# Kernel optimization log

Hardware: AMD Instinct MI355X
Metric: run time of the kernel (lower is better)

Reference implementation:

```python
import jax, jax.numpy as jnp
import numpy as np

B, T, L = 4096, 26, 4      # batch, num sparse tables, bag size (multi-hot)
N_ROWS, M = 100000, 64     # rows per table, embedding dim
LN_BOT = [13, 512, 256, 64]
LN_TOP = [415, 512, 256, 1]


def _mlp_params(key, ln):
    Ws, bs = [], []
    for i in range(len(ln) - 1):
        n, m = ln[i], ln[i + 1]
        key, k1, k2 = jax.random.split(key, 3)
        Ws.append(jax.random.normal(k1, (m, n), jnp.float32) * np.sqrt(2.0 / (m + n)))
        bs.append(jax.random.normal(k2, (m,), jnp.float32) * np.sqrt(1.0 / m))
    return Ws, bs


def setup_inputs() -> dict:
    key = jax.random.key(0)
    k_dense, k_idx, k_emb, k_bot, k_top = jax.random.split(key, 5)
    dense_x = jax.random.normal(k_dense, (B, LN_BOT[0]), jnp.float32)
    sparse_idx = jax.random.randint(k_idx, (B, T, L), 0, N_ROWS, jnp.int64 if jax.config.jax_enable_x64 else jnp.int32)
    # per-table uniform init U(-1/sqrt(n), 1/sqrt(n)); all tables same size -> stacked
    bound = np.sqrt(1.0 / N_ROWS)
    emb_tables = jax.random.uniform(k_emb, (T, N_ROWS, M), jnp.float32, -bound, bound)
    bw, bb = _mlp_params(k_bot, LN_BOT)
    tw, tb = _mlp_params(k_top, LN_TOP)
    return {
        "dense_x": dense_x, "sparse_idx": sparse_idx, "emb_tables": emb_tables,
        "bot_W0": bw[0], "bot_b0": bb[0], "bot_W1": bw[1], "bot_b1": bb[1],
        "bot_W2": bw[2], "bot_b2": bb[2],
        "top_W0": tw[0], "top_b0": tb[0], "top_W1": tw[1], "top_b1": tb[1],
        "top_W2": tw[2], "top_b2": tb[2],
    }


def _dlrm_forward(dense_x, sparse_idx, emb_tables, bot, top):
    # bottom MLP (all ReLU; sigmoid_layer index not hit for bottom)
    x = dense_x
    for W, b in bot:
        x = jax.nn.relu(x @ W.T + b)                       # [B, 64] at the end
    # apply_emb: per-table EmbeddingBag(mode='sum'): gather L rows, sum-pool
    # emb_tables: [T, N, M], sparse_idx: [B, T, L] -> E: [B, T, M]
    E = jax.vmap(lambda tab, ix: tab[ix].sum(axis=1), in_axes=(0, 1), out_axes=1)(
        emb_tables, sparse_idx)
    # dot interaction: concat bottom output with pooled embeddings
    Tcat = jnp.concatenate([x[:, None, :], E], axis=1)     # [B, T+1, M]
    Z = jnp.einsum("bim,bjm->bij", Tcat, Tcat)             # [B, T+1, T+1]
    li, lj = np.tril_indices(T + 1, k=-1)                  # strictly lower triangle
    Zflat = Z[:, li, lj]                                   # [B, (T+1)T/2]
    R = jnp.concatenate([x, Zflat], axis=1)                # [B, 415]
    # top MLP: ReLU hidden, Sigmoid on last layer
    h = R
    for i, (W, b) in enumerate(top):
        h = h @ W.T + b
        h = jax.nn.sigmoid(h) if i == len(top) - 1 else jax.nn.relu(h)
    return h                                               # [B, 1]


def reference(dense_x, sparse_idx, emb_tables,
              bot_W0, bot_b0, bot_W1, bot_b1, bot_W2, bot_b2,
              top_W0, top_b0, top_W1, top_b1, top_W2, top_b2):
    bot = [(bot_W0, bot_b0), (bot_W1, bot_b1), (bot_W2, bot_b2)]
    top = [(top_W0, top_b0), (top_W1, top_b1), (top_W2, top_b2)]
    return _dlrm_forward(dense_x, sparse_idx, emb_tables, bot, top)
```

## Files before the change

### kernel.cpp

```cpp
#include <hip/hip_runtime.h>
#include <hip/hip_bf16.h>
#include <cstddef>
#include <cstdint>

#define BATCH 4096
#define TT 26
#define LL 4
#define NROWS 100000
#define MM 64
#define RSTR 512

typedef __attribute__((ext_vector_type(8))) short bf16x8;
typedef __attribute__((ext_vector_type(4))) float f32x4;
typedef __attribute__((ext_vector_type(16))) float f32x16;

#define AS1 __attribute__((address_space(1)))
#define AS3 __attribute__((address_space(3)))

__device__ __forceinline__ void gload_lds16(const void* g, void* l) {
    __builtin_amdgcn_global_load_lds((const AS1 unsigned int*)g,
                                     (AS3 unsigned int*)l, 16, 0, 0);
}

__device__ __forceinline__ float bu2f(unsigned short u) {
    unsigned int x = (unsigned int)u << 16;
    float f; __builtin_memcpy(&f, &x, 4); return f;
}

#define GATB 4096
#define BOT0B 8192
__global__ __launch_bounds__(256) void fused_front_kernel(
    const int* __restrict__ idx, const float* __restrict__ emb,
    const float* __restrict__ dense, const float* __restrict__ bw0,
    const float* __restrict__ bb0,
    const float* __restrict__ bw1, const float* __restrict__ bw2,
    const float* __restrict__ tw0, const float* __restrict__ tw1,
    unsigned short* __restrict__ E, __hip_bfloat16* __restrict__ x1,
    __hip_bfloat16* __restrict__ bw1b, __hip_bfloat16* __restrict__ bw2b,
    __hip_bfloat16* __restrict__ tw0b, __hip_bfloat16* __restrict__ tw1b)
{
    __shared__ int sidx[TT * LL];
    __shared__ float xr[13];
    const int tid = threadIdx.x;

    if (blockIdx.x < GATB) {
        const int b = blockIdx.x;
        const int lane = tid & 63;
        const int w = tid >> 6;
        if (tid < TT * LL) sidx[tid] = idx[(size_t)b * (TT * LL) + tid];
        __syncthreads();
        float v[7][4];
#pragma unroll
        for (int rr = 0; rr < 7; rr++) {
            int t = rr * 4 + w;
            if (t < TT) {
                const float* tab = emb + (size_t)t * NROWS * MM + lane;
#pragma unroll
                for (int l = 0; l < LL; l++)
                    v[rr][l] = tab[(size_t)sidx[t * LL + l] * MM];
            }
        }
#pragma unroll
        for (int rr = 0; rr < 7; rr++) {
            int t = rr * 4 + w;
            if (t < TT) {
                float s = v[rr][0] + v[rr][1] + v[rr][2] + v[rr][3];
                __hip_bfloat16 hv = __float2bfloat16(s);
                E[(size_t)b * (TT * MM) + t * MM + lane] = *(unsigned short*)&hv;
            }
        }
        return;
    }
    if (blockIdx.x < BOT0B) {
        const int b = blockIdx.x - GATB;
        if (tid < 13) xr[tid] = dense[b * 13 + tid];
        __syncthreads();
        for (int j = tid; j < 512; j += 256) {
            const float* w = bw0 + j * 13;
            float s = bb0[j];
#pragma unroll
            for (int k = 0; k < 13; k++) s = fmaf(xr[k], w[k], s);
            x1[(size_t)b * 512 + j] = __float2bfloat16(fmaxf(s, 0.f));
        }
        return;
    }
    {
        int i = (blockIdx.x - BOT0B) * 256 + tid;
        if (i < 131072) {
            bw1b[i] = __float2bfloat16(bw1[i]);
        } else if (i < 147456) {
            int j = i - 131072; bw2b[j] = __float2bfloat16(bw2[j]);
        } else if (i < 409600) {
            int j = i - 147456; int n = j >> 9, k = j & 511;
            tw0b[j] = __float2bfloat16(k < 415 ? tw0[n * 415 + k] : 0.f);
        } else if (i < 540672) {
            int j = i - 409600; tw1b[j] = __float2bfloat16(tw1[j]);
        }
    }
}

template<int KK, int ACT>
__global__ __launch_bounds__(256, 2) void gemm_db(
    const __hip_bfloat16* __restrict__ A,
    const __hip_bfloat16* __restrict__ W,
    const float* __restrict__ bias,
    __hip_bfloat16* __restrict__ C, int ldc)
{
    constexpr int KSTEPS = KK / 128;
    __shared__ __align__(16) short As[2][64 * 128];
    __shared__ __align__(16) short Bs[2][64 * 128];

    const int tid  = threadIdx.x;
    const int lane = tid & 63;
    const int wid  = tid >> 6;
    const int wr   = wid >> 1, wc = wid & 1;

    const char* Ab = (const char*)A + (size_t)blockIdx.x * (64 * KK * 2);
    const char* Wb = (const char*)W + (size_t)blockIdx.y * (64 * KK * 2);

    auto stage = [&](const char* Gb, char* Ls, int ks) {
#pragma unroll
        for (int j = 0; j < 4; j++) {
            int ci  = j * 256 + tid;
            int row = ci >> 4;
            int cb  = (ci & 15) * 16;
            int src = row * (2 * KK) + ks * 256 + (cb ^ ((row & 7) << 4));
            gload_lds16(Gb + src, Ls + row * 256 + cb);
        }
    };

    const int fr  = lane & 15;
    const int fkb = (lane >> 4) * 16;
    const int xrr = (fr & 7) << 4;
    const int oA0 = (wr * 32 + fr) * 256;
    const int oA1 = oA0 + 16 * 256;
    const int oB0 = (wc * 32 + fr) * 256;
    const int oB1 = oB0 + 16 * 256;

    f32x4 acc[2][2] = {};

    auto compute = [&](const char* Ah, const char* Bh) {
#pragma unroll
        for (int kf = 0; kf < 4; kf++) {
            int pc = (kf * 64 + fkb) ^ xrr;
            bf16x8 a0 = *(const bf16x8*)(Ah + oA0 + pc);
            bf16x8 a1 = *(const bf16x8*)(Ah + oA1 + pc);
            bf16x8 b0 = *(const bf16x8*)(Bh + oB0 + pc);
            bf16x8 b1 = *(const bf16x8*)(Bh + oB1 + pc);
            acc[0][0] = __builtin_amdgcn_mfma_f32_16x16x32_bf16(a0, b0, acc[0][0], 0, 0, 0);
            acc[0][1] = __builtin_amdgcn_mfma_f32_16x16x32_bf16(a0, b1, acc[0][1], 0, 0, 0);
            acc[1][0] = __builtin_amdgcn_mfma_f32_16x16x32_bf16(a1, b0, acc[1][0], 0, 0, 0);
            acc[1][1] = __builtin_amdgcn_mfma_f32_16x16x32_bf16(a1, b1, acc[1][1], 0, 0, 0);
        }
    };

    stage(Ab, (char*)As[0], 0); stage(Wb, (char*)Bs[0], 0);
    stage(Ab, (char*)As[1], 1); stage(Wb, (char*)Bs[1], 1);

#pragma unroll
    for (int ks = 0; ks < KSTEPS; ks++) {
        if (ks < KSTEPS - 1) { asm volatile("s_waitcnt vmcnt(8)" ::: "memory"); }
        else                 { asm volatile("s_waitcnt vmcnt(0)" ::: "memory"); }
        __builtin_amdgcn_sched_barrier(0);
        __builtin_amdgcn_s_barrier();
        __builtin_amdgcn_sched_barrier(0);
        compute((const char*)As[ks & 1], (const char*)Bs[ks & 1]);
        __builtin_amdgcn_sched_barrier(0);
        if (ks + 2 < KSTEPS) {
            __builtin_amdgcn_s_barrier();
            stage(Ab, (char*)As[ks & 1], ks + 2);
            stage(Wb, (char*)Bs[ks & 1], ks + 2);
        }
    }

    const int col0 = blockIdx.y * 64 + wc * 32 + (lane & 15);
    const int row0 = blockIdx.x * 64 + wr * 32 + (lane >> 4) * 4;
    float bias_n0 = bias[col0];
    float bias_n1 = bias[col0 + 16];
#pragma unroll
    for (int mi = 0; mi < 2; mi++) {
#pragma unroll
        for (int j = 0; j < 4; j++) {
            int row = row0 + mi * 16 + j;
            float v0 = acc[mi][0][j] + bias_n0;
            float v1 = acc[mi][1][j] + bias_n1;
            if (ACT == 1) { v0 = fmaxf(v0, 0.f); v1 = fmaxf(v1, 0.f); }
            C[(size_t)row * ldc + col0]      = __float2bfloat16(v0);
            C[(size_t)row * ldc + col0 + 16] = __float2bfloat16(v1);
        }
    }
}

__global__ __launch_bounds__(256) void interact_kernel(
    const unsigned short* __restrict__ E, __hip_bfloat16* __restrict__ R)
{
    __shared__ __align__(16) char T[4][32 * 128];
    const int tid = threadIdx.x;
    const int lane = tid & 63;
    const int w = tid >> 6;
    const int b = blockIdx.x * 4 + w;
    char* Tw = T[w];
    const unsigned short* Eb = E + (size_t)b * (TT * MM);
    const unsigned short* Xb = (const unsigned short*)R + (size_t)b * RSTR;

#pragma unroll
    for (int i = 0; i < 7; i++) {
        int id = i * 64 + lane;
        if (id < 432) {
            int r = id >> 4, c4 = (id & 15) * 4;
            const unsigned short* src = (r == 0) ? (Xb + c4) : (Eb + (r - 1) * 64 + c4);
            ushort4 val = *(const ushort4*)src;
            *(ushort4*)(Tw + r * 128 + ((c4 * 2) ^ ((r & 7) << 4))) = val;
        }
    }
#pragma unroll
    for (int i = 0; i < 2; i++) {
        int id = i * 64 + lane;
        if (id < 80) {
            int r = 27 + (id >> 4), c4 = (id & 15) * 4;
            *(ushort4*)(Tw + r * 128 + ((c4 * 2) ^ ((r & 7) << 4))) = (ushort4){0, 0, 0, 0};
        }
    }
    __syncthreads();

    f32x16 acc = {};
#pragma unroll
    for (int m = 0; m < 4; m++) {
        int byteoff = (lane & 31) * 128 + ((m * 32 + (lane >> 5) * 16) ^ ((lane & 7) << 4));
        bf16x8 f = *(const bf16x8*)(Tw + byteoff);
        acc = __builtin_amdgcn_mfma_f32_32x32x16_bf16(f, f, acc, 0, 0, 0);
    }
    __hip_bfloat16* Rb = R + (size_t)b * RSTR;
    const int col = lane & 31;
#pragma unroll
    for (int q = 0; q < 4; q++) {
#pragma unroll
        for (int j = 0; j < 4; j++) {
            int row = j + 8 * q + 4 * (lane >> 5);
            if (row < 27 && col < row)
                Rb[64 + row * (row - 1) / 2 + col] = __float2bfloat16(acc[q * 4 + j]);
        }
    }
    for (int p = lane; p < 97; p += 64)
        Rb[415 + p] = __float2bfloat16(0.f);
}

__global__ __launch_bounds__(256) void top2_kernel(
    const __hip_bfloat16* __restrict__ h, const float* __restrict__ W,
    const float* __restrict__ bias, float* __restrict__ out)
{
    __shared__ float ws[256];
    int tid = threadIdx.x;
    ws[tid] = W[tid];
    __syncthreads();
    int b = blockIdx.x * 4 + (tid >> 6);
    int lane = tid & 63;
    const unsigned short* hb = (const unsigned short*)(h + (size_t)b * 256);
    ushort4 hv = *(const ushort4*)&hb[lane * 4];
    float4 wv = *(const float4*)&ws[lane * 4];
    float s = bu2f(hv.x) * wv.x + bu2f(hv.y) * wv.y + bu2f(hv.z) * wv.z + bu2f(hv.w) * wv.w;
#pragma unroll
    for (int off = 32; off >= 1; off >>= 1)
        s += __shfl_xor(s, off, 64);
    if (lane == 0) {
        float v = s + bias[0];
        out[b] = 1.0f / (1.0f + expf(-v));
    }
}

extern "C" void kernel_launch(void* const* d_in, const int* in_sizes, int n_in,
                              void* d_out, int out_size, void* d_ws, size_t ws_size,
                              hipStream_t stream) {
    const float* dense = (const float*)d_in[0];
    const int*   sidx  = (const int*)d_in[1];
    const float* emb   = (const float*)d_in[2];
    const float* bw0   = (const float*)d_in[3];
    const float* bb0   = (const float*)d_in[4];
    const float* bw1   = (const float*)d_in[5];
    const float* bb1   = (const float*)d_in[6];
    const float* bw2   = (const float*)d_in[7];
    const float* bb2   = (const float*)d_in[8];
    const float* tw0   = (const float*)d_in[9];
    const float* tb0   = (const float*)d_in[10];
    const float* tw1   = (const float*)d_in[11];
    const float* tb1   = (const float*)d_in[12];
    const float* tw2   = (const float*)d_in[13];
    const float* tb2   = (const float*)d_in[14];
    float* out = (float*)d_out;

    char* wsb = (char*)d_ws;
    unsigned short* E    = (unsigned short*)(wsb);
    __hip_bfloat16* R    = (__hip_bfloat16*)(wsb + (16u << 20));
    __hip_bfloat16* h1   = (__hip_bfloat16*)(wsb + (20u << 20));
    __hip_bfloat16* h2   = (__hip_bfloat16*)(wsb + (24u << 20));
    __hip_bfloat16* x1   = (__hip_bfloat16*)(wsb + (26u << 20));
    __hip_bfloat16* x2   = (__hip_bfloat16*)(wsb + (30u << 20));
    __hip_bfloat16* bw1b = (__hip_bfloat16*)(wsb + (32u << 20));
    __hip_bfloat16* bw2b = bw1b + 131072;
    __hip_bfloat16* tw0b = bw2b + 16384;
    __hip_bfloat16* tw1b = tw0b + 262144;

    fused_front_kernel<<<GATB + BATCH + 2112, 256, 0, stream>>>(
        sidx, emb, dense, bw0, bb0, bw1, bw2, tw0, tw1,
        E, x1, bw1b, bw2b, tw0b, tw1b);

    gemm_db<512, 1><<<dim3(64, 4), 256, 0, stream>>>(x1, bw1b, bb1, x2, 256);

    gemm_db<256, 1><<<dim3(64, 1), 256, 0, stream>>>(x2, bw2b, bb2, R, RSTR);

    interact_kernel<<<BATCH / 4, 256, 0, stream>>>(E, R);

    gemm_db<512, 1><<<dim3(64, 8), 256, 0, stream>>>(R, tw0b, tb0, h1, 512);

    gemm_db<512, 1><<<dim3(64, 4), 256, 0, stream>>>(h1, tw1b, tb1, h2, 256);

    top2_kernel<<<BATCH / 4, 256, 0, stream>>>(h2, tw2, tb2, out);
}
```

Measured before the change: 56.79 us.

## Fuse embedding Gram into gather, fuse bottom-MLP tail with x-dot products, full-K GEMMs

The gather blocks now stage the pooled embeddings in LDS and compute the embedding-embedding dot products with one MFMA wave, writing them directly into R. The last bottom-MLP GEMM also computes the x·E dot products from LDS, so the separate interaction kernel is gone. Two GEMMs switch to a full-K variant that stages all of K into LDS up front with two barriers instead of a K loop. Together these remove a kernel launch and a re-read of E from global memory. In exchange the gather blocks use more LDS and barriers, the bottom GEMM runs on only 64 blocks, and the larger full-K LDS footprint may lower occupancy.

```diff
diff --git a/kernel.cpp b/kernel.cpp
--- a/kernel.cpp
+++ b/kernel.cpp
@@ -37,8 +37,10 @@
     const float* __restrict__ tw0, const float* __restrict__ tw1,
     unsigned short* __restrict__ E, __hip_bfloat16* __restrict__ x1,
     __hip_bfloat16* __restrict__ bw1b, __hip_bfloat16* __restrict__ bw2b,
-    __hip_bfloat16* __restrict__ tw0b, __hip_bfloat16* __restrict__ tw1b)
+    __hip_bfloat16* __restrict__ tw0b, __hip_bfloat16* __restrict__ tw1b,
+    __hip_bfloat16* __restrict__ R)
 {
+    __shared__ __align__(16) char T[32 * 128];
     __shared__ int sidx[TT * LL];
     __shared__ float xr[13];
     const int tid = threadIdx.x;
@@ -48,7 +50,14 @@
         const int lane = tid & 63;
         const int w = tid >> 6;
         if (tid < TT * LL) sidx[tid] = idx[(size_t)b * (TT * LL) + tid];
+        for (int i = tid; i < 6 * 64; i += 256) {
+            int rid = i >> 6;
+            int r = rid ? (26 + rid) : 0;
+            int l = i & 63;
+            *(short*)(T + r * 128 + ((l * 2) ^ ((r & 7) << 4))) = 0;
+        }
         __syncthreads();
+
         float v[7][4];
 #pragma unroll
         for (int rr = 0; rr < 7; rr++) {
@@ -66,7 +75,36 @@
             if (t < TT) {
                 float s = v[rr][0] + v[rr][1] + v[rr][2] + v[rr][3];
                 __hip_bfloat16 hv = __float2bfloat16(s);
+                int r = t + 1;
+                *(short*)(T + r * 128 + ((lane * 2) ^ ((r & 7) << 4))) = *(short*)&hv;
                 E[(size_t)b * (TT * MM) + t * MM + lane] = *(unsigned short*)&hv;
+            }
+        }
+        __syncthreads();
+
+        __hip_bfloat16* Rb = R + (size_t)b * RSTR;
+        if (w == 1) {
+            Rb[415 + lane] = __float2bfloat16(0.f);
+            if (lane < 33) Rb[479 + lane] = __float2bfloat16(0.f);
+        }
+        if (w == 0) {
+            f32x16 acc = {};
+#pragma unroll
+            for (int m = 0; m < 4; m++) {
+                int byteoff = (lane & 31) * 128 +
+                              ((m * 32 + (lane >> 5) * 16) ^ ((lane & 7) << 4));
+                bf16x8 f = *(const bf16x8*)(T + byteoff);
+                acc = __builtin_amdgcn_mfma_f32_32x32x16_bf16(f, f, acc, 0, 0, 0);
+            }
+            const int col = lane & 31;
+#pragma unroll
+            for (int q = 0; q < 4; q++) {
+#pragma unroll
+                for (int j = 0; j < 4; j++) {
+                    int row = j + 8 * q + 4 * (lane >> 5);
+                    if (row < 27 && col >= 1 && col < row)
+                        Rb[64 + row * (row - 1) / 2 + col] = __float2bfloat16(acc[q * 4 + j]);
+                }
             }
         }
         return;
@@ -95,6 +133,211 @@
             tw0b[j] = __float2bfloat16(k < 415 ? tw0[n * 415 + k] : 0.f);
         } else if (i < 540672) {
             int j = i - 409600; tw1b[j] = __float2bfloat16(tw1[j]);
+        }
+    }
+}
+
+template<int KK, int ACT>
+__global__ __launch_bounds__(256) void gemm_fullk(
+    const __hip_bfloat16* __restrict__ A,
+    const __hip_bfloat16* __restrict__ W,
+    const float* __restrict__ bias,
+    __hip_bfloat16* __restrict__ C, int ldc)
+{
+    constexpr int HS   = KK / 2;
+    constexpr int CPRH = KK / 16;
+    constexpr int NI   = (64 * CPRH) / 256;
+    __shared__ __align__(16) short As0[64 * HS];
+    __shared__ __align__(16) short As1[64 * HS];
+    __shared__ __align__(16) short Bs0[64 * HS];
+    __shared__ __align__(16) short Bs1[64 * HS];
+
+    const int tid  = threadIdx.x;
+    const int lane = tid & 63;
+    const int wid  = tid >> 6;
+    const int wr   = wid >> 1, wc = wid & 1;
+
+    const char* Ab = (const char*)A + (size_t)blockIdx.x * (64 * KK * 2);
+    const char* Wb = (const char*)W + (size_t)blockIdx.y * (64 * KK * 2);
+
+    auto stage = [&](const char* Gb, short* Ls, int h) {
+#pragma unroll
+        for (int j = 0; j < NI; j++) {
+            int ci  = j * 256 + tid;
+            int row = ci / CPRH;
+            int cb  = (ci & (CPRH - 1)) * 16;
+            int src = row * (2 * KK) + h * KK + (cb ^ ((row & 7) << 4));
+            gload_lds16(Gb + src, (char*)Ls + row * KK + cb);
+        }
+    };
+    stage(Ab, As0, 0); stage(Wb, Bs0, 0);
+    stage(Ab, As1, 1); stage(Wb, Bs1, 1);
+
+    const int frow = lane & 15;
+    const int fkb  = (lane >> 4) * 16;
+    const int xr   = (frow & 7) << 4;
+    const int oA0  = (wr * 32 + frow) * KK;
+    const int oA1  = oA0 + 16 * KK;
+    const int oB0  = (wc * 32 + frow) * KK;
+    const int oB1  = oB0 + 16 * KK;
+
+    f32x4 acc[2][2] = {};
+
+    auto compute = [&](const short* Ah, const short* Bh) {
+#pragma unroll
+        for (int ks = 0; ks < KK / 64; ks++) {
+            int pc = (ks * 64 + fkb) ^ xr;
+            bf16x8 a0 = *(const bf16x8*)((const char*)Ah + oA0 + pc);
+            bf16x8 a1 = *(const bf16x8*)((const char*)Ah + oA1 + pc);
+            bf16x8 b0 = *(const bf16x8*)((const char*)Bh + oB0 + pc);
+            bf16x8 b1 = *(const bf16x8*)((const char*)Bh + oB1 + pc);
+            acc[0][0] = __builtin_amdgcn_mfma_f32_16x16x32_bf16(a0, b0, acc[0][0], 0, 0, 0);
+            acc[0][1] = __builtin_amdgcn_mfma_f32_16x16x32_bf16(a0, b1, acc[0][1], 0, 0, 0);
+            acc[1][0] = __builtin_amdgcn_mfma_f32_16x16x32_bf16(a1, b0, acc[1][0], 0, 0, 0);
+            acc[1][1] = __builtin_amdgcn_mfma_f32_16x16x32_bf16(a1, b1, acc[1][1], 0, 0, 0);
+        }
+    };
+
+    asm volatile("s_waitcnt vmcnt(%0)" :: "i"(2 * NI) : "memory");
+    __builtin_amdgcn_sched_barrier(0);
+    __builtin_amdgcn_s_barrier();
+    __builtin_amdgcn_sched_barrier(0);
+    compute(As0, Bs0);
+    asm volatile("s_waitcnt vmcnt(0)" ::: "memory");
+    __builtin_amdgcn_sched_barrier(0);
+    __builtin_amdgcn_s_barrier();
+    __builtin_amdgcn_sched_barrier(0);
+    compute(As1, Bs1);
+
+    const int col0 = blockIdx.y * 64 + wc * 32 + (lane & 15);
+    const int row0 = blockIdx.x * 64 + wr * 32 + (lane >> 4) * 4;
+    float bias_n0 = bias[col0];
+    float bias_n1 = bias[col0 + 16];
+#pragma unroll
+    for (int mi = 0; mi < 2; mi++) {
+#pragma unroll
+        for (int j = 0; j < 4; j++) {
+            int row = row0 + mi * 16 + j;
+            float v0 = acc[mi][0][j] + bias_n0;
+            float v1 = acc[mi][1][j] + bias_n1;
+            if (ACT == 1) { v0 = fmaxf(v0, 0.f); v1 = fmaxf(v1, 0.f); }
+            C[(size_t)row * ldc + col0]      = __float2bfloat16(v0);
+            C[(size_t)row * ldc + col0 + 16] = __float2bfloat16(v1);
+        }
+    }
+}
+
+__global__ __launch_bounds__(256) void bot2_gram_kernel(
+    const __hip_bfloat16* __restrict__ A,
+    const __hip_bfloat16* __restrict__ W,
+    const float* __restrict__ bias,
+    const unsigned short* __restrict__ E,
+    __hip_bfloat16* __restrict__ R)
+{
+    constexpr int KK = 256;
+    __shared__ __align__(16) short As0[64 * 128];
+    __shared__ __align__(16) short As1[64 * 128];
+    __shared__ __align__(16) short Bs0[64 * 128];
+    __shared__ __align__(16) short Bs1[64 * 128];
+    __shared__ unsigned short x3L[64 * 64];
+
+    const int tid  = threadIdx.x;
+    const int lane = tid & 63;
+    const int wid  = tid >> 6;
+    const int wr   = wid >> 1, wc = wid & 1;
+
+    const char* Ab = (const char*)A + (size_t)blockIdx.x * (64 * KK * 2);
+    const char* Wb = (const char*)W;
+
+    auto stage = [&](const char* Gb, short* Ls, int h) {
+#pragma unroll
+        for (int j = 0; j < 4; j++) {
+            int ci  = j * 256 + tid;
+            int row = ci >> 4;
+            int cb  = (ci & 15) * 16;
+            int src = row * (2 * KK) + h * KK + (cb ^ ((row & 7) << 4));
+            gload_lds16(Gb + src, (char*)Ls + row * KK + cb);
+        }
+    };
+    stage(Ab, As0, 0); stage(Wb, Bs0, 0);
+    stage(Ab, As1, 1); stage(Wb, Bs1, 1);
+
+    const int frow = lane & 15;
+    const int fkb  = (lane >> 4) * 16;
+    const int xr   = (frow & 7) << 4;
+    const int oA0  = (wr * 32 + frow) * KK;
+    const int oA1  = oA0 + 16 * KK;
+    const int oB0  = (wc * 32 + frow) * KK;
+    const int oB1  = oB0 + 16 * KK;
+
+    f32x4 acc[2][2] = {};
+    auto compute = [&](const short* Ah, const short* Bh) {
+#pragma unroll
+        for (int ks = 0; ks < KK / 64; ks++) {
+            int pc = (ks * 64 + fkb) ^ xr;
+            bf16x8 a0 = *(const bf16x8*)((const char*)Ah + oA0 + pc);
+            bf16x8 a1 = *(const bf16x8*)((const char*)Ah + oA1 + pc);
+            bf16x8 b0 = *(const bf16x8*)((const char*)Bh + oB0 + pc);
+            bf16x8 b1 = *(const bf16x8*)((const char*)Bh + oB1 + pc);
+            acc[0][0] = __builtin_amdgcn_mfma_f32_16x16x32_bf16(a0, b0, acc[0][0], 0, 0, 0);
+            acc[0][1] = __builtin_amdgcn_mfma_f32_16x16x32_bf16(a0, b1, acc[0][1], 0, 0, 0);
+            acc[1][0] = __builtin_amdgcn_mfma_f32_16x16x32_bf16(a1, b0, acc[1][0], 0, 0, 0);
+            acc[1][1] = __builtin_amdgcn_mfma_f32_16x16x32_bf16(a1, b1, acc[1][1], 0, 0, 0);
+        }
+    };
+
+    asm volatile("s_waitcnt vmcnt(8)" ::: "memory");
+    __builtin_amdgcn_sched_barrier(0);
+    __builtin_amdgcn_s_barrier();
+    __builtin_amdgcn_sched_barrier(0);
+    compute(As0, Bs0);
+    asm volatile("s_waitcnt vmcnt(0)" ::: "memory");
+    __builtin_amdgcn_sched_barrier(0);
+    __builtin_amdgcn_s_barrier();
+    __builtin_amdgcn_sched_barrier(0);
+    compute(As1, Bs1);
+
+    const int col0 = wc * 32 + (lane & 15);
+    const int lrow0 = wr * 32 + (lane >> 4) * 4;
+    const int row0 = blockIdx.x * 64 + lrow0;
+    float bias_n0 = bias[col0];
+    float bias_n1 = bias[col0 + 16];
+#pragma unroll
+    for (int mi = 0; mi < 2; mi++) {
+#pragma unroll
+        for (int j = 0; j < 4; j++) {
+            int row = row0 + mi * 16 + j;
+            int lr  = lrow0 + mi * 16 + j;
+            float v0 = fmaxf(acc[mi][0][j] + bias_n0, 0.f);
+            float v1 = fmaxf(acc[mi][1][j] + bias_n1, 0.f);
+            __hip_bfloat16 h0 = __float2bfloat16(v0);
+            __hip_bfloat16 h1 = __float2bfloat16(v1);
+            R[(size_t)row * RSTR + col0]      = h0;
+            R[(size_t)row * RSTR + col0 + 16] = h1;
+            x3L[lr * 64 + col0]      = *(unsigned short*)&h0;
+            x3L[lr * 64 + col0 + 16] = *(unsigned short*)&h1;
+        }
+    }
+    __syncthreads();
+
+    const int b0 = blockIdx.x * 64;
+#pragma unroll
+    for (int k = 0; k < 7; k++) {
+        int job = tid + k * 256;
+        if (job < 1664) {
+            int bl = job / 26;
+            int i  = job - bl * 26 + 1;
+            const unsigned short* Er = E + ((size_t)(b0 + bl) * TT + (i - 1)) * MM;
+            const unsigned short* xrow = &x3L[bl * 64];
+            float s = 0.f;
+#pragma unroll
+            for (int c = 0; c < 64; c += 4) {
+                ushort4 e4 = *(const ushort4*)&Er[c];
+                ushort4 x4 = *(const ushort4*)&xrow[c];
+                s += bu2f(e4.x) * bu2f(x4.x) + bu2f(e4.y) * bu2f(x4.y)
+                   + bu2f(e4.z) * bu2f(x4.z) + bu2f(e4.w) * bu2f(x4.w);
+            }
+            R[(size_t)(b0 + bl) * RSTR + 64 + i * (i - 1) / 2] = __float2bfloat16(s);
         }
     }
 }
@@ -189,60 +432,6 @@
             C[(size_t)row * ldc + col0 + 16] = __float2bfloat16(v1);
         }
     }
-}
-
-__global__ __launch_bounds__(256) void interact_kernel(
-    const unsigned short* __restrict__ E, __hip_bfloat16* __restrict__ R)
-{
-    __shared__ __align__(16) char T[4][32 * 128];
-    const int tid = threadIdx.x;
-    const int lane = tid & 63;
-    const int w = tid >> 6;
-    const int b = blockIdx.x * 4 + w;
-    char* Tw = T[w];
-    const unsigned short* Eb = E + (size_t)b * (TT * MM);
-    const unsigned short* Xb = (const unsigned short*)R + (size_t)b * RSTR;
-
-#pragma unroll
-    for (int i = 0; i < 7; i++) {
-        int id = i * 64 + lane;
-        if (id < 432) {
-            int r = id >> 4, c4 = (id & 15) * 4;
-            const unsigned short* src = (r == 0) ? (Xb + c4) : (Eb + (r - 1) * 64 + c4);
-            ushort4 val = *(const ushort4*)src;
-            *(ushort4*)(Tw + r * 128 + ((c4 * 2) ^ ((r & 7) << 4))) = val;
-        }
-    }
-#pragma unroll
-    for (int i = 0; i < 2; i++) {
-        int id = i * 64 + lane;
-        if (id < 80) {
-            int r = 27 + (id >> 4), c4 = (id & 15) * 4;
-            *(ushort4*)(Tw + r * 128 + ((c4 * 2) ^ ((r & 7) << 4))) = (ushort4){0, 0, 0, 0};
-        }
-    }
-    __syncthreads();
-
-    f32x16 acc = {};
-#pragma unroll
-    for (int m = 0; m < 4; m++) {
-        int byteoff = (lane & 31) * 128 + ((m * 32 + (lane >> 5) * 16) ^ ((lane & 7) << 4));
-        bf16x8 f = *(const bf16x8*)(Tw + byteoff);
-        acc = __builtin_amdgcn_mfma_f32_32x32x16_bf16(f, f, acc, 0, 0, 0);
-    }
-    __hip_bfloat16* Rb = R + (size_t)b * RSTR;
-    const int col = lane & 31;
-#pragma unroll
-    for (int q = 0; q < 4; q++) {
-#pragma unroll
-        for (int j = 0; j < 4; j++) {
-            int row = j + 8 * q + 4 * (lane >> 5);
-            if (row < 27 && col < row)
-                Rb[64 + row * (row - 1) / 2 + col] = __float2bfloat16(acc[q * 4 + j]);
-        }
-    }
-    for (int p = lane; p < 97; p += 64)
-        Rb[415 + p] = __float2bfloat16(0.f);
 }
 
 __global__ __launch_bounds__(256) void top2_kernel(
@@ -302,17 +491,15 @@
 
     fused_front_kernel<<<GATB + BATCH + 2112, 256, 0, stream>>>(
         sidx, emb, dense, bw0, bb0, bw1, bw2, tw0, tw1,
-        E, x1, bw1b, bw2b, tw0b, tw1b);
-
-    gemm_db<512, 1><<<dim3(64, 4), 256, 0, stream>>>(x1, bw1b, bb1, x2, 256);
-
-    gemm_db<256, 1><<<dim3(64, 1), 256, 0, stream>>>(x2, bw2b, bb2, R, RSTR);
-
-    interact_kernel<<<BATCH / 4, 256, 0, stream>>>(E, R);
+        E, x1, bw1b, bw2b, tw0b, tw1b, R);
+
+    gemm_fullk<512, 1><<<dim3(64, 4), 256, 0, stream>>>(x1, bw1b, bb1, x2, 256);
+
+    bot2_gram_kernel<<<64, 256, 0, stream>>>(x2, bw2b, bb2, E, R);
 
     gemm_db<512, 1><<<dim3(64, 8), 256, 0, stream>>>(R, tw0b, tb0, h1, 512);
 
-    gemm_db<512, 1><<<dim3(64, 4), 256, 0, stream>>>(h1, tw1b, tb1, h2, 256);
+    gemm_fullk<512, 1><<<dim3(64, 4), 256, 0, stream>>>(h1, tw1b, tb1, h2, 256);
 
     top2_kernel<<<BATCH / 4, 256, 0, stream>>>(h2, tw2, tb2, out);
 }
```

Result: slower. 59.17 us (+4.2%).

## Add full-K single-shot GEMM kernel staging whole K into LDS in two halves

Applied to the files above, without the earlier changes.

Introduces gemm_fullk, which issues async global-to-LDS loads for the entire K extent of A and W tiles up front, split into two halves. It computes on the first half while the second is still landing, replacing the k-step double-buffered loop of gemm_db. This is applied to three of the small MLP GEMMs. It aims to cut per-k-step barrier and loop overhead for these short GEMMs, at the cost of much larger LDS use (128KB for K=512), which lowers occupancy.

```diff
diff --git a/kernel.cpp b/kernel.cpp
--- a/kernel.cpp
+++ b/kernel.cpp
@@ -95,6 +95,96 @@
             tw0b[j] = __float2bfloat16(k < 415 ? tw0[n * 415 + k] : 0.f);
         } else if (i < 540672) {
             int j = i - 409600; tw1b[j] = __float2bfloat16(tw1[j]);
+        }
+    }
+}
+
+template<int KK, int ACT>
+__global__ __launch_bounds__(256) void gemm_fullk(
+    const __hip_bfloat16* __restrict__ A,
+    const __hip_bfloat16* __restrict__ W,
+    const float* __restrict__ bias,
+    __hip_bfloat16* __restrict__ C, int ldc)
+{
+    constexpr int HS   = KK / 2;
+    constexpr int CPRH = KK / 16;
+    constexpr int NI   = (64 * CPRH) / 256;
+    __shared__ __align__(16) short As0[64 * HS];
+    __shared__ __align__(16) short As1[64 * HS];
+    __shared__ __align__(16) short Bs0[64 * HS];
+    __shared__ __align__(16) short Bs1[64 * HS];
+
+    const int tid  = threadIdx.x;
+    const int lane = tid & 63;
+    const int wid  = tid >> 6;
+    const int wr   = wid >> 1, wc = wid & 1;
+
+    const char* Ab = (const char*)A + (size_t)blockIdx.x * (64 * KK * 2);
+    const char* Wb = (const char*)W + (size_t)blockIdx.y * (64 * KK * 2);
+
+    auto stage = [&](const char* Gb, short* Ls, int h) {
+#pragma unroll
+        for (int j = 0; j < NI; j++) {
+            int ci  = j * 256 + tid;
+            int row = ci / CPRH;
+            int cb  = (ci & (CPRH - 1)) * 16;
+            int src = row * (2 * KK) + h * KK + (cb ^ ((row & 7) << 4));
+            gload_lds16(Gb + src, (char*)Ls + row * KK + cb);
+        }
+    };
+    stage(Ab, As0, 0); stage(Wb, Bs0, 0);
+    stage(Ab, As1, 1); stage(Wb, Bs1, 1);
+
+    const int frow = lane & 15;
+    const int fkb  = (lane >> 4) * 16;
+    const int xr   = (frow & 7) << 4;
+    const int oA0  = (wr * 32 + frow) * KK;
+    const int oA1  = oA0 + 16 * KK;
+    const int oB0  = (wc * 32 + frow) * KK;
+    const int oB1  = oB0 + 16 * KK;
+
+    f32x4 acc[2][2] = {};
+
+    auto compute = [&](const short* Ah, const short* Bh) {
+#pragma unroll
+        for (int ks = 0; ks < KK / 64; ks++) {
+            int pc = (ks * 64 + fkb) ^ xr;
+            bf16x8 a0 = *(const bf16x8*)((const char*)Ah + oA0 + pc);
+            bf16x8 a1 = *(const bf16x8*)((const char*)Ah + oA1 + pc);
+            bf16x8 b0 = *(const bf16x8*)((const char*)Bh + oB0 + pc);
+            bf16x8 b1 = *(const bf16x8*)((const char*)Bh + oB1 + pc);
+            acc[0][0] = __builtin_amdgcn_mfma_f32_16x16x32_bf16(a0, b0, acc[0][0], 0, 0, 0);
+            acc[0][1] = __builtin_amdgcn_mfma_f32_16x16x32_bf16(a0, b1, acc[0][1], 0, 0, 0);
+            acc[1][0] = __builtin_amdgcn_mfma_f32_16x16x32_bf16(a1, b0, acc[1][0], 0, 0, 0);
+            acc[1][1] = __builtin_amdgcn_mfma_f32_16x16x32_bf16(a1, b1, acc[1][1], 0, 0, 0);
+        }
+    };
+
+    asm volatile("s_waitcnt vmcnt(%0)" :: "i"(2 * NI) : "memory");
+    __builtin_amdgcn_sched_barrier(0);
+    __builtin_amdgcn_s_barrier();
+    __builtin_amdgcn_sched_barrier(0);
+    compute(As0, Bs0);
+    asm volatile("s_waitcnt vmcnt(0)" ::: "memory");
+    __builtin_amdgcn_sched_barrier(0);
+    __builtin_amdgcn_s_barrier();
+    __builtin_amdgcn_sched_barrier(0);
+    compute(As1, Bs1);
+
+    const int col0 = blockIdx.y * 64 + wc * 32 + (lane & 15);
+    const int row0 = blockIdx.x * 64 + wr * 32 + (lane >> 4) * 4;
+    float bias_n0 = bias[col0];
+    float bias_n1 = bias[col0 + 16];
+#pragma unroll
+    for (int mi = 0; mi < 2; mi++) {
+#pragma unroll
+        for (int j = 0; j < 4; j++) {
+            int row = row0 + mi * 16 + j;
+            float v0 = acc[mi][0][j] + bias_n0;
+            float v1 = acc[mi][1][j] + bias_n1;
+            if (ACT == 1) { v0 = fmaxf(v0, 0.f); v1 = fmaxf(v1, 0.f); }
+            C[(size_t)row * ldc + col0]      = __float2bfloat16(v0);
+            C[(size_t)row * ldc + col0 + 16] = __float2bfloat16(v1);
         }
     }
 }
@@ -304,15 +394,15 @@
         sidx, emb, dense, bw0, bb0, bw1, bw2, tw0, tw1,
         E, x1, bw1b, bw2b, tw0b, tw1b);
 
-    gemm_db<512, 1><<<dim3(64, 4), 256, 0, stream>>>(x1, bw1b, bb1, x2, 256);
-
-    gemm_db<256, 1><<<dim3(64, 1), 256, 0, stream>>>(x2, bw2b, bb2, R, RSTR);
+    gemm_fullk<512, 1><<<dim3(64, 4), 256, 0, stream>>>(x1, bw1b, bb1, x2, 256);
+
+    gemm_fullk<256, 1><<<dim3(64, 1), 256, 0, stream>>>(x2, bw2b, bb2, R, RSTR);
 
     interact_kernel<<<BATCH / 4, 256, 0, stream>>>(E, R);
 
     gemm_db<512, 1><<<dim3(64, 8), 256, 0, stream>>>(R, tw0b, tb0, h1, 512);
 
-    gemm_db<512, 1><<<dim3(64, 4), 256, 0, stream>>>(h1, tw1b, tb1, h2, 256);
+    gemm_fullk<512, 1><<<dim3(64, 4), 256, 0, stream>>>(h1, tw1b, tb1, h2, 256);
 
     top2_kernel<<<BATCH / 4, 256, 0, stream>>>(h2, tw2, tb2, out);
 }
```

Measured after the change: 56.00 us. About the same (-1.4%).
